# Kernel optimization log

Measured on AMD Instinct MI355X. Metric: run time of the kernel, lower is better.

Reference implementation:

```python
import jax, jax.numpy as jnp
import numpy as np

EPS = 1e-8  # torch.nn.CosineSimilarity default eps


def setup_inputs() -> dict:
    key = jax.random.key(0)
    # [N maps, B batch, C, H, W] saliency tensors
    sal = jax.random.normal(key, (8, 32, 3, 224, 224), dtype=jnp.float32)
    return {"sal_tensor_list": sal}


def reference(sal_tensor_list):
    N, B = sal_tensor_list.shape[0], sal_tensor_list.shape[1]
    x = sal_tensor_list.reshape(N, B, -1)              # [N, B, D]
    # pairwise batched dot products: Gram over maps, per batch element
    dots = jnp.einsum('ibd,jbd->ijb', x, x)            # [N, N, B]
    norms = jnp.sqrt(jnp.sum(x * x, axis=-1))          # [N, B]
    denom = jnp.maximum(norms[:, None, :] * norms[None, :, :], EPS)
    pair_mean = jnp.abs(dots / denom).mean(axis=-1)    # [N, N] mean over batch
    # only combinations i < j (upper triangle, no diagonal)
    mask = jnp.triu(jnp.ones((N, N), dtype=bool), k=1)
    n_pairs = N * (N - 1) // 2
    return jnp.sum(jnp.where(mask, pair_mean, 0.0)) / n_pairs
```

## Files before the change

### kernel.cpp

```cpp
#include <hip/hip_runtime.h>

#define NMAPS 8
#define BATCH 32
#define DLEN  150528
#define D4    (DLEN / 4)
#define NPAIR 36
#define CHUNKS 32
#define TPB   256
#define JSTRIDE (CHUNKS * TPB)

__global__ __launch_bounds__(TPB) void gram_kernel(const float* __restrict__ x,
                                                   float* __restrict__ partial) {
    const int b     = blockIdx.x;
    const int chunk = blockIdx.y;
    const int tid   = threadIdx.x;

    const float4* xb = reinterpret_cast<const float4*>(x) + (size_t)b * D4;
    const size_t strideI = (size_t)BATCH * D4;

    float acc[NPAIR];
#pragma unroll
    for (int k = 0; k < NPAIR; ++k) acc[k] = 0.0f;

    int j = chunk * TPB + tid;
    float4 v[NMAPS], w[NMAPS];
#pragma unroll
    for (int i = 0; i < NMAPS; ++i) v[i] = xb[(size_t)i * strideI + j];

    for (int j2 = j + JSTRIDE; j2 < D4; j2 += JSTRIDE) {
#pragma unroll
        for (int i = 0; i < NMAPS; ++i) w[i] = xb[(size_t)i * strideI + j2];
        int k = 0;
#pragma unroll
        for (int i = 0; i < NMAPS; ++i) {
#pragma unroll
            for (int jj = i; jj < NMAPS; ++jj) {
                acc[k] += v[i].x * v[jj].x + v[i].y * v[jj].y +
                          v[i].z * v[jj].z + v[i].w * v[jj].w;
                ++k;
            }
        }
#pragma unroll
        for (int i = 0; i < NMAPS; ++i) v[i] = w[i];
    }
    {
        int k = 0;
#pragma unroll
        for (int i = 0; i < NMAPS; ++i) {
#pragma unroll
            for (int jj = i; jj < NMAPS; ++jj) {
                acc[k] += v[i].x * v[jj].x + v[i].y * v[jj].y +
                          v[i].z * v[jj].z + v[i].w * v[jj].w;
                ++k;
            }
        }
    }

    const int lane = tid & 63;
    const int wave = tid >> 6;
    __shared__ float red[TPB / 64][NPAIR];
#pragma unroll
    for (int k = 0; k < NPAIR; ++k) {
        float s = acc[k];
#pragma unroll
        for (int off = 32; off > 0; off >>= 1) s += __shfl_down(s, off, 64);
        if (lane == 0) red[wave][k] = s;
    }
    __syncthreads();
    if (tid < NPAIR) {
        partial[chunk * (BATCH * NPAIR) + b * NPAIR + tid] =
            red[0][tid] + red[1][tid] + red[2][tid] + red[3][tid];
    }
}

__global__ __launch_bounds__(256) void finalize_kernel(const float* __restrict__ partial,
                                                       float* __restrict__ out) {
    const int tid = threadIdx.x;
    __shared__ float dots_s[BATCH * NPAIR];
    __shared__ float norms[BATCH][NMAPS];

    for (int item = tid; item < BATCH * NPAIR; item += 256) {
        float s = 0.0f;
#pragma unroll
        for (int c = 0; c < CHUNKS; ++c) s += partial[c * (BATCH * NPAIR) + item];
        dots_s[item] = s;
    }
    __syncthreads();
    {
        int b = tid >> 3, i = tid & 7;
        int diag = 8 * i - (i * (i - 1)) / 2;
        norms[b][i] = sqrtf(dots_s[b * NPAIR + diag]);
    }
    __syncthreads();

    float sum = 0.0f;
    for (int item = tid; item < 28 * BATCH; item += 256) {
        int p = item >> 5;
        int b = item & 31;
        int i = 0, rem = p;
        while (rem >= 7 - i) { rem -= 7 - i; ++i; }
        int j = i + 1 + rem;
        int k = 8 * i - (i * (i - 1)) / 2 + (j - i);
        float d   = fabsf(dots_s[b * NPAIR + k]);
        float den = fmaxf(norms[b][i] * norms[b][j], 1e-8f);
        sum += d / den;
    }

    const int lane = tid & 63, wave = tid >> 6;
    __shared__ float red[4];
#pragma unroll
    for (int off = 32; off > 0; off >>= 1) sum += __shfl_down(sum, off, 64);
    if (lane == 0) red[wave] = sum;
    __syncthreads();
    if (tid == 0) {
        out[0] = (red[0] + red[1] + red[2] + red[3]) / (28.0f * BATCH);
    }
}

extern "C" void kernel_launch(void* const* d_in, const int* in_sizes, int n_in,
                              void* d_out, int out_size, void* d_ws, size_t ws_size,
                              hipStream_t stream) {
    const float* x       = (const float*)d_in[0];
    float*       out     = (float*)d_out;
    float*       partial = (float*)d_ws;

    dim3 grid(BATCH, CHUNKS);
    gram_kernel<<<grid, TPB, 0, stream>>>(x, partial);
    finalize_kernel<<<1, 256, 0, stream>>>(partial, out);
}
```

Before: 41.36 us.

## Use contiguous per-chunk float2 regions with 512-thread blocks in Gram kernel

```diff
diff --git a/kernel.cpp b/kernel.cpp
--- a/kernel.cpp
+++ b/kernel.cpp
@@ -3,58 +3,51 @@
 #define NMAPS 8
 #define BATCH 32
 #define DLEN  150528
-#define D4    (DLEN / 4)
+#define D2    (DLEN / 2)
 #define NPAIR 36
 #define CHUNKS 32
-#define TPB   256
-#define JSTRIDE (CHUNKS * TPB)
+#define TPB   512
+#define REG2  (D2 / CHUNKS)
+#define FULL_ITERS (REG2 / TPB)
+#define TAIL  (REG2 - FULL_ITERS * TPB)
 
-__global__ __launch_bounds__(TPB) void gram_kernel(const float* __restrict__ x,
-                                                   float* __restrict__ partial) {
+__device__ __forceinline__ void gram_step(const float2* __restrict__ base,
+                                          size_t strideI, size_t j,
+                                          float acc[NPAIR]) {
+    float2 v[NMAPS];
+#pragma unroll
+    for (int i = 0; i < NMAPS; ++i) v[i] = base[(size_t)i * strideI + j];
+    int k = 0;
+#pragma unroll
+    for (int i = 0; i < NMAPS; ++i) {
+#pragma unroll
+        for (int jj = i; jj < NMAPS; ++jj) {
+            acc[k] += v[i].x * v[jj].x + v[i].y * v[jj].y;
+            ++k;
+        }
+    }
+}
+
+__global__ __launch_bounds__(TPB, 8) void gram_kernel(const float* __restrict__ xf,
+                                                      float* __restrict__ partial) {
     const int b     = blockIdx.x;
     const int chunk = blockIdx.y;
     const int tid   = threadIdx.x;
 
-    const float4* xb = reinterpret_cast<const float4*>(x) + (size_t)b * D4;
-    const size_t strideI = (size_t)BATCH * D4;
+    const float2* xb = reinterpret_cast<const float2*>(xf) + (size_t)b * D2;
+    const size_t strideI = (size_t)BATCH * D2;
 
     float acc[NPAIR];
 #pragma unroll
     for (int k = 0; k < NPAIR; ++k) acc[k] = 0.0f;
 
-    int j = chunk * TPB + tid;
-    float4 v[NMAPS], w[NMAPS];
-#pragma unroll
-    for (int i = 0; i < NMAPS; ++i) v[i] = xb[(size_t)i * strideI + j];
+    const size_t j0 = (size_t)chunk * REG2 + tid;
 
-    for (int j2 = j + JSTRIDE; j2 < D4; j2 += JSTRIDE) {
-#pragma unroll
-        for (int i = 0; i < NMAPS; ++i) w[i] = xb[(size_t)i * strideI + j2];
-        int k = 0;
-#pragma unroll
-        for (int i = 0; i < NMAPS; ++i) {
-#pragma unroll
-            for (int jj = i; jj < NMAPS; ++jj) {
-                acc[k] += v[i].x * v[jj].x + v[i].y * v[jj].y +
-                          v[i].z * v[jj].z + v[i].w * v[jj].w;
-                ++k;
-            }
-        }
-#pragma unroll
-        for (int i = 0; i < NMAPS; ++i) v[i] = w[i];
-    }
-    {
-        int k = 0;
-#pragma unroll
-        for (int i = 0; i < NMAPS; ++i) {
-#pragma unroll
-            for (int jj = i; jj < NMAPS; ++jj) {
-                acc[k] += v[i].x * v[jj].x + v[i].y * v[jj].y +
-                          v[i].z * v[jj].z + v[i].w * v[jj].w;
-                ++k;
-            }
-        }
-    }
+#pragma unroll 1
+    for (int it = 0; it < FULL_ITERS; ++it)
+        gram_step(xb, strideI, j0 + (size_t)it * TPB, acc);
+    if (tid < TAIL)
+        gram_step(xb, strideI, j0 + (size_t)FULL_ITERS * TPB, acc);
 
     const int lane = tid & 63;
     const int wave = tid >> 6;
@@ -68,8 +61,10 @@
     }
     __syncthreads();
     if (tid < NPAIR) {
-        partial[chunk * (BATCH * NPAIR) + b * NPAIR + tid] =
-            red[0][tid] + red[1][tid] + red[2][tid] + red[3][tid];
+        float t = 0.0f;
+#pragma unroll
+        for (int w = 0; w < TPB / 64; ++w) t += red[w][tid];
+        partial[((size_t)b * NPAIR + tid) * CHUNKS + chunk] = t;
     }
 }
 
@@ -80,41 +75,44 @@
     __shared__ float norms[BATCH][NMAPS];
 
     for (int item = tid; item < BATCH * NPAIR; item += 256) {
+        const float4* p = reinterpret_cast<const float4*>(partial + (size_t)item * CHUNKS);
         float s = 0.0f;
 #pragma unroll
-        for (int c = 0; c < CHUNKS; ++c) s += partial[c * (BATCH * NPAIR) + item];
+        for (int c = 0; c < CHUNKS / 4; ++c) {
+            float4 t = p[c];
+            s += t.x + t.y + t.z + t.w;
+        }
         dots_s[item] = s;
     }
     __syncthreads();
     {
-        int b = tid >> 3, i = tid & 7;
+        int bb = tid >> 3, i = tid & 7;
         int diag = 8 * i - (i * (i - 1)) / 2;
-        norms[b][i] = sqrtf(dots_s[b * NPAIR + diag]);
+        norms[bb][i] = sqrtf(dots_s[bb * NPAIR + diag]);
     }
     __syncthreads();
 
     float sum = 0.0f;
     for (int item = tid; item < 28 * BATCH; item += 256) {
         int p = item >> 5;
-        int b = item & 31;
+        int bb = item & 31;
         int i = 0, rem = p;
         while (rem >= 7 - i) { rem -= 7 - i; ++i; }
         int j = i + 1 + rem;
         int k = 8 * i - (i * (i - 1)) / 2 + (j - i);
-        float d   = fabsf(dots_s[b * NPAIR + k]);
-        float den = fmaxf(norms[b][i] * norms[b][j], 1e-8f);
+        float d   = fabsf(dots_s[bb * NPAIR + k]);
+        float den = fmaxf(norms[bb][i] * norms[bb][j], 1e-8f);
         sum += d / den;
     }
 
     const int lane = tid & 63, wave = tid >> 6;
-    __shared__ float red[4];
+    __shared__ float red2[4];
 #pragma unroll
     for (int off = 32; off > 0; off >>= 1) sum += __shfl_down(sum, off, 64);
-    if (lane == 0) red[wave] = sum;
+    if (lane == 0) red2[wave] = sum;
     __syncthreads();
-    if (tid == 0) {
-        out[0] = (red[0] + red[1] + red[2] + red[3]) / (28.0f * BATCH);
-    }
+    if (tid == 0)
+        out[0] = (red2[0] + red2[1] + red2[2] + red2[3]) / (28.0f * BATCH);
 }
 
 extern "C" void kernel_launch(void* const* d_in, const int* in_sizes, int n_in,
```

Result: slower. 56.92 us (+37.6%).
